# Optimization experiments

Hardware: AMD Instinct MI355X
Metric: run time of the kernel (lower is better)

Reference implementation:

```python
import jax, jax.numpy as jnp
import numpy as np

N_NODES = 50000


def gcn_conv(x, edge_index, W, b):
    """PyG-style GCNConv: add self-loops, symmetric normalization, x@W + bias."""
    N = x.shape[0]
    loop = jnp.arange(N, dtype=edge_index.dtype)
    src = jnp.concatenate([edge_index[0], loop])  # message sources
    dst = jnp.concatenate([edge_index[1], loop])  # aggregation targets
    deg = jax.ops.segment_sum(jnp.ones_like(dst, dtype=x.dtype), dst, num_segments=N)
    dinv = jnp.where(deg > 0, jax.lax.rsqrt(jnp.maximum(deg, 1.0)), 0.0)
    norm = dinv[src] * dinv[dst]  # [E+N]
    h = x @ W  # [N, out] dense transform first (fewer edge-dim FLOPs)
    msg = h[src] * norm[:, None]  # [E+N, out] gathered, normalized messages
    out = jax.ops.segment_sum(msg, dst, num_segments=N)
    return out + b


def setup_inputs() -> dict:
    key = jax.random.key(0)
    k1, k2, k3, k4 = jax.random.split(key, 4)
    x = jax.random.normal(k1, (N_NODES, 256), dtype=jnp.float32)
    edge_index = jax.random.randint(k2, (2, 800000), 0, N_NODES, dtype=jnp.int64)
    W1 = jax.random.normal(k3, (256, 256), dtype=jnp.float32) * (1.0 / np.sqrt(256))
    b1 = jnp.zeros((256,), dtype=jnp.float32)
    W2 = jax.random.normal(k4, (256, 128), dtype=jnp.float32) * (1.0 / np.sqrt(256))
    b2 = jnp.zeros((128,), dtype=jnp.float32)
    return {"x": x, "edge_index": edge_index, "W1": W1, "b1": b1, "W2": W2, "b2": b2}


def reference(x, edge_index, W1, b1, W2, b2):
    h = gcn_conv(x, edge_index, W1, b1)
    h = jax.nn.relu(h)
    return gcn_conv(h, edge_index, W2, b2)
```

## Files before the change

### kernel.cpp

```cpp
#include <hip/hip_runtime.h>

#define N_FEAT_IN 256
#define N_HID 256
#define N_OUT 128

using f32x4 = __attribute__((ext_vector_type(4))) float;
using bf16x8 = __attribute__((ext_vector_type(8))) short;

__device__ inline unsigned short bf16_rne(float f) {
    unsigned u = __builtin_bit_cast(unsigned, f);
    unsigned r = u + 0x7FFFu + ((u >> 16) & 1u);
    return (unsigned short)(r >> 16);
}
__device__ inline float bf16_to_f(unsigned short h) {
    unsigned u = ((unsigned)h) << 16;
    return __builtin_bit_cast(float, u);
}

__global__ void detect_i64_kernel(const int* __restrict__ edges, int* __restrict__ flag) {
    __shared__ int s[256];
    int tid = threadIdx.x;
    int zeros = 0;
    for (int i = tid; i < 2048; i += 256) zeros += (edges[2 * i + 1] == 0) ? 1 : 0;
    s[tid] = zeros;
    __syncthreads();
    for (int off = 128; off; off >>= 1) {
        if (tid < off) s[tid] += s[tid + off];
        __syncthreads();
    }
    if (tid == 0) flag[0] = (s[0] > 1900) ? 1 : 0;
}

__global__ void count_kernel(const void* __restrict__ edges, int E,
                             const int* __restrict__ flag, int* __restrict__ cnt) {
    int e = blockIdx.x * blockDim.x + threadIdx.x;
    if (e >= E) return;
    int d;
    if (flag[0]) {
        d = (int)((const long long*)edges)[(size_t)E + e];
    } else {
        d = ((const int*)edges)[(size_t)E + e];
    }
    atomicAdd(&cnt[d], 1);
}

__global__ __launch_bounds__(256) void scan_block_kernel(
    const int* __restrict__ cnt, int Nn, int* __restrict__ rowp, int* __restrict__ bsum,
    float* __restrict__ dinv) {
    __shared__ int sd[256];
    const int tid = threadIdx.x;
    const int i = blockIdx.x * 256 + tid;
    const int v = (i < Nn) ? cnt[i] : 0;
    if (i < Nn) dinv[i] = rsqrtf((float)(v + 1));
    sd[tid] = v;
    __syncthreads();
    for (int off = 1; off < 256; off <<= 1) {
        int t = (tid >= off) ? sd[tid - off] : 0;
        __syncthreads();
        sd[tid] += t;
        __syncthreads();
    }
    if (i < Nn) rowp[i] = sd[tid] - v;
    if (tid == 255) bsum[blockIdx.x] = sd[255];
}

__global__ __launch_bounds__(256) void scan_top_kernel(
    int* __restrict__ bsum, int Nb, int* __restrict__ rowp, int Nn) {
    __shared__ int sd[256];
    const int tid = threadIdx.x;
    const int v = (tid < Nb) ? bsum[tid] : 0;
    sd[tid] = v;
    __syncthreads();
    for (int off = 1; off < 256; off <<= 1) {
        int t = (tid >= off) ? sd[tid - off] : 0;
        __syncthreads();
        sd[tid] += t;
        __syncthreads();
    }
    if (tid < Nb) bsum[tid] = sd[tid] - v;
    if (tid == 255) rowp[Nn] = sd[255];
}

__global__ __launch_bounds__(256) void scan_add_kernel(
    const int* __restrict__ bsum, int Nn, int* __restrict__ rowp, int* __restrict__ cursor) {
    const int i = blockIdx.x * 256 + threadIdx.x;
    if (i < Nn) {
        const int r = rowp[i] + bsum[i >> 8];
        rowp[i] = r;
        cursor[i] = r;
    }
}

__global__ void fill_kernel(const void* __restrict__ edges, int E,
                            const int* __restrict__ flag,
                            const float* __restrict__ dinv, int* __restrict__ cursor,
                            int2* __restrict__ ce) {
    int e = blockIdx.x * blockDim.x + threadIdx.x;
    if (e >= E) return;
    int s, d;
    if (flag[0]) {
        const long long* p = (const long long*)edges;
        s = (int)p[e];
        d = (int)p[(size_t)E + e];
    } else {
        const int* p = (const int*)edges;
        s = p[e];
        d = p[(size_t)E + e];
    }
    int pos = atomicAdd(&cursor[d], 1);
    float w = dinv[s] * dinv[d];
    ce[pos] = make_int2(s, __builtin_bit_cast(int, w));
}

__global__ __launch_bounds__(256) void splitT_kernel(
    const float* __restrict__ W, int K, int N,
    unsigned short* __restrict__ thi, unsigned short* __restrict__ tlo) {
    int idx = blockIdx.x * 256 + threadIdx.x;
    if (idx >= K * N) return;
    int k = idx / N, n = idx - k * N;
    float f = W[idx];
    unsigned short h = bf16_rne(f);
    unsigned short l = bf16_rne(f - bf16_to_f(h));
    thi[(size_t)n * K + k] = h;
    tlo[(size_t)n * K + k] = l;
}

__global__ __launch_bounds__(256) void gemm_mfma_f32a_kernel(
    const float* __restrict__ Af,
    const unsigned short* __restrict__ Bh, const unsigned short* __restrict__ Bl,
    unsigned short* __restrict__ C, int M, int N, int K) {
    __shared__ char lds[4 * 128 * 64];
    char* As_h = lds;
    char* As_l = lds + 8192;
    char* Bs_h = lds + 16384;
    char* Bs_l = lds + 24576;

    const int tid = threadIdx.x;
    const int lane = tid & 63;
    const int wv = tid >> 6;
    const int wrow = (wv >> 1) * 64;
    const int wcol = (wv & 1) * 64;

    const int srow = tid >> 1;
    const int shalf = tid & 1;

    const long arow_g = (long)blockIdx.y * 128 + srow;
    const bool aval = arow_g < M;
    const int bcol_g = blockIdx.x * 128 + srow;

    const size_t a_base = (size_t)(aval ? arow_g : 0) * K + shalf * 16;
    const size_t b_base = (size_t)bcol_g * K + shalf * 16;

    const int sw = ((srow >> 1) & 3) << 4;
    const int w0 = (srow * 64 + shalf * 32) ^ sw;
    const int w1 = (srow * 64 + shalf * 32 + 16) ^ sw;

    int ra[4], rb[4];
#pragma unroll
    for (int m = 0; m < 4; m++) {
        int r = wrow + m * 16 + (lane & 15);
        ra[m] = (r * 64 + (lane >> 4) * 16) ^ (((r >> 1) & 3) << 4);
        int c = wcol + m * 16 + (lane & 15);
        rb[m] = (c * 64 + (lane >> 4) * 16) ^ (((c >> 1) & 3) << 4);
    }

    f32x4 acc[4][4] = {};

    const int nkt = K >> 5;
    for (int kt = 0; kt < nkt; kt++) {
        const int kb = kt * 32;
        float fa[16];
#pragma unroll
        for (int i = 0; i < 16; i++) fa[i] = 0.f;
        if (aval) {
#pragma unroll
            for (int i = 0; i < 4; i++) {
                float4 f = *(const float4*)(Af + a_base + kb + i * 4);
                fa[i * 4 + 0] = f.x; fa[i * 4 + 1] = f.y;
                fa[i * 4 + 2] = f.z; fa[i * 4 + 3] = f.w;
            }
        }
        bf16x8 vah0, vah1, val0, val1;
#pragma unroll
        for (int i = 0; i < 8; i++) {
            unsigned short hh = bf16_rne(fa[i]);
            unsigned short ll = bf16_rne(fa[i] - bf16_to_f(hh));
            vah0[i] = (short)hh; val0[i] = (short)ll;
            unsigned short hh1 = bf16_rne(fa[8 + i]);
            unsigned short ll1 = bf16_rne(fa[8 + i] - bf16_to_f(hh1));
            vah1[i] = (short)hh1; val1[i] = (short)ll1;
        }
        bf16x8 vbh0 = *(const bf16x8*)(Bh + b_base + kb);
        bf16x8 vbh1 = *(const bf16x8*)(Bh + b_base + kb + 8);
        bf16x8 vbl0 = *(const bf16x8*)(Bl + b_base + kb);
        bf16x8 vbl1 = *(const bf16x8*)(Bl + b_base + kb + 8);
        __syncthreads();
        *(bf16x8*)(As_h + w0) = vah0;  *(bf16x8*)(As_h + w1) = vah1;
        *(bf16x8*)(As_l + w0) = val0;  *(bf16x8*)(As_l + w1) = val1;
        *(bf16x8*)(Bs_h + w0) = vbh0;  *(bf16x8*)(Bs_h + w1) = vbh1;
        *(bf16x8*)(Bs_l + w0) = vbl0;  *(bf16x8*)(Bs_l + w1) = vbl1;
        __syncthreads();
        bf16x8 ah[4], al[4], bh[4], bl[4];
#pragma unroll
        for (int m = 0; m < 4; m++) {
            ah[m] = *(const bf16x8*)(As_h + ra[m]);
            al[m] = *(const bf16x8*)(As_l + ra[m]);
            bh[m] = *(const bf16x8*)(Bs_h + rb[m]);
            bl[m] = *(const bf16x8*)(Bs_l + rb[m]);
        }
#pragma unroll
        for (int m = 0; m < 4; m++)
#pragma unroll
            for (int n = 0; n < 4; n++) {
                acc[m][n] = __builtin_amdgcn_mfma_f32_16x16x32_bf16(ah[m], bh[n], acc[m][n], 0, 0, 0);
                acc[m][n] = __builtin_amdgcn_mfma_f32_16x16x32_bf16(al[m], bh[n], acc[m][n], 0, 0, 0);
                acc[m][n] = __builtin_amdgcn_mfma_f32_16x16x32_bf16(ah[m], bl[n], acc[m][n], 0, 0, 0);
            }
    }

    const int c0 = blockIdx.x * 128 + wcol + (lane & 15);
    const long r0 = (long)blockIdx.y * 128 + wrow + (lane >> 4) * 4;
#pragma unroll
    for (int m = 0; m < 4; m++)
#pragma unroll
        for (int j = 0; j < 4; j++) {
            long r = r0 + m * 16 + j;
            if (r < M) {
#pragma unroll
                for (int n = 0; n < 4; n++)
                    C[(size_t)r * N + c0 + n * 16] = bf16_rne(acc[m][n][j]);
            }
        }
}

__global__ __launch_bounds__(256) void gemm_mfma_kernel(
    const unsigned short* __restrict__ Ah, const unsigned short* __restrict__ Al,
    const unsigned short* __restrict__ Bh, const unsigned short* __restrict__ Bl,
    unsigned short* __restrict__ C, int M, int N, int K) {
    __shared__ char lds[4 * 128 * 64];
    char* As_h = lds;
    char* As_l = lds + 8192;
    char* Bs_h = lds + 16384;
    char* Bs_l = lds + 24576;

    const int tid = threadIdx.x;
    const int lane = tid & 63;
    const int wv = tid >> 6;
    const int wrow = (wv >> 1) * 64;
    const int wcol = (wv & 1) * 64;

    const int srow = tid >> 1;
    const int shalf = tid & 1;

    const long arow_g = (long)blockIdx.y * 128 + srow;
    const bool aval = arow_g < M;
    const int bcol_g = blockIdx.x * 128 + srow;

    const size_t a_base = (size_t)(aval ? arow_g : 0) * K + shalf * 16;
    const size_t b_base = (size_t)bcol_g * K + shalf * 16;

    const int sw = ((srow >> 1) & 3) << 4;
    const int w0 = (srow * 64 + shalf * 32) ^ sw;
    const int w1 = (srow * 64 + shalf * 32 + 16) ^ sw;

    int ra[4], rb[4];
#pragma unroll
    for (int m = 0; m < 4; m++) {
        int r = wrow + m * 16 + (lane & 15);
        ra[m] = (r * 64 + (lane >> 4) * 16) ^ (((r >> 1) & 3) << 4);
        int c = wcol + m * 16 + (lane & 15);
        rb[m] = (c * 64 + (lane >> 4) * 16) ^ (((c >> 1) & 3) << 4);
    }

    f32x4 acc[4][4] = {};
    const bf16x8 zero8 = {0, 0, 0, 0, 0, 0, 0, 0};

    const int nkt = K >> 5;
    for (int kt = 0; kt < nkt; kt++) {
        const int kb = kt * 32;
        bf16x8 vah0 = zero8, vah1 = zero8, val0 = zero8, val1 = zero8;
        if (aval) {
            vah0 = *(const bf16x8*)(Ah + a_base + kb);
            vah1 = *(const bf16x8*)(Ah + a_base + kb + 8);
            val0 = *(const bf16x8*)(Al + a_base + kb);
            val1 = *(const bf16x8*)(Al + a_base + kb + 8);
        }
        bf16x8 vbh0 = *(const bf16x8*)(Bh + b_base + kb);
        bf16x8 vbh1 = *(const bf16x8*)(Bh + b_base + kb + 8);
        bf16x8 vbl0 = *(const bf16x8*)(Bl + b_base + kb);
        bf16x8 vbl1 = *(const bf16x8*)(Bl + b_base + kb + 8);
        __syncthreads();
        *(bf16x8*)(As_h + w0) = vah0;  *(bf16x8*)(As_h + w1) = vah1;
        *(bf16x8*)(As_l + w0) = val0;  *(bf16x8*)(As_l + w1) = val1;
        *(bf16x8*)(Bs_h + w0) = vbh0;  *(bf16x8*)(Bs_h + w1) = vbh1;
        *(bf16x8*)(Bs_l + w0) = vbl0;  *(bf16x8*)(Bs_l + w1) = vbl1;
        __syncthreads();
        bf16x8 ah[4], al[4], bh[4], bl[4];
#pragma unroll
        for (int m = 0; m < 4; m++) {
            ah[m] = *(const bf16x8*)(As_h + ra[m]);
            al[m] = *(const bf16x8*)(As_l + ra[m]);
            bh[m] = *(const bf16x8*)(Bs_h + rb[m]);
            bl[m] = *(const bf16x8*)(Bs_l + rb[m]);
        }
#pragma unroll
        for (int m = 0; m < 4; m++)
#pragma unroll
            for (int n = 0; n < 4; n++) {
                acc[m][n] = __builtin_amdgcn_mfma_f32_16x16x32_bf16(ah[m], bh[n], acc[m][n], 0, 0, 0);
                acc[m][n] = __builtin_amdgcn_mfma_f32_16x16x32_bf16(al[m], bh[n], acc[m][n], 0, 0, 0);
                acc[m][n] = __builtin_amdgcn_mfma_f32_16x16x32_bf16(ah[m], bl[n], acc[m][n], 0, 0, 0);
            }
    }

    const int c0 = blockIdx.x * 128 + wcol + (lane & 15);
    const long r0 = (long)blockIdx.y * 128 + wrow + (lane >> 4) * 4;
#pragma unroll
    for (int m = 0; m < 4; m++)
#pragma unroll
        for (int j = 0; j < 4; j++) {
            long r = r0 + m * 16 + j;
            if (r < M) {
#pragma unroll
                for (int n = 0; n < 4; n++)
                    C[(size_t)r * N + c0 + n * 16] = bf16_rne(acc[m][n][j]);
            }
        }
}

template <int C, bool RELU, bool SPLIT>
__global__ __launch_bounds__(256) void agg_kernel(
    const unsigned short* __restrict__ h, const int* __restrict__ rowp,
    const int2* __restrict__ ce,
    const float* __restrict__ dinv, const float* __restrict__ bias,
    float* __restrict__ out,
    unsigned short* __restrict__ ohi, unsigned short* __restrict__ olo, int Nn) {
    constexpr int VEC = C / 64;
    static_assert(VEC == 2 || VEC == 4, "C must be 128 or 256");
    const int lane = threadIdx.x & 63;
    const int wv = threadIdx.x >> 6;
    const int node0 = blockIdx.x * 4 + wv;
    if (node0 >= Nn) return;
    const int node = __builtin_amdgcn_readfirstlane(node0);
    const float di = dinv[node];
    const int coff = lane * VEC;
    const unsigned short* __restrict__ hc = h + coff;
    float acc[VEC];

    auto loadrow = [&](int row, float v[VEC]) {
        const unsigned short* r = hc + (size_t)row * C;
        if constexpr (VEC == 4) {
            ushort4 t = *(const ushort4*)r;
            v[0] = bf16_to_f(t.x); v[1] = bf16_to_f(t.y);
            v[2] = bf16_to_f(t.z); v[3] = bf16_to_f(t.w);
        } else {
            ushort2 t = *(const ushort2*)r;
            v[0] = bf16_to_f(t.x); v[1] = bf16_to_f(t.y);
        }
    };

    {
        float v[VEC];
        loadrow(node, v);
#pragma unroll
        for (int j = 0; j < VEC; j++) acc[j] = di * di * v[j];
    }

    const int s = rowp[node];
    const int e = rowp[node + 1];
    for (int base = s; base < e; base += 64) {
        const int m = min(64, e - base);
        int myc = 0, myn = 0;
        if (lane < m) {
            int2 p = ce[base + lane];
            myc = p.x;
            myn = p.y;
        }
        int j = 0;
        for (; j + 4 <= m; j += 4) {
            const int c0 = __builtin_amdgcn_readlane(myc, j);
            const int c1 = __builtin_amdgcn_readlane(myc, j + 1);
            const int c2 = __builtin_amdgcn_readlane(myc, j + 2);
            const int c3 = __builtin_amdgcn_readlane(myc, j + 3);
            const float w0 = __builtin_bit_cast(float, __builtin_amdgcn_readlane(myn, j));
            const float w1 = __builtin_bit_cast(float, __builtin_amdgcn_readlane(myn, j + 1));
            const float w2 = __builtin_bit_cast(float, __builtin_amdgcn_readlane(myn, j + 2));
            const float w3 = __builtin_bit_cast(float, __builtin_amdgcn_readlane(myn, j + 3));
            float v0[VEC], v1[VEC], v2[VEC], v3[VEC];
            loadrow(c0, v0);
            loadrow(c1, v1);
            loadrow(c2, v2);
            loadrow(c3, v3);
#pragma unroll
            for (int q = 0; q < VEC; q++)
                acc[q] += w0 * v0[q] + w1 * v1[q] + w2 * v2[q] + w3 * v3[q];
        }
        for (; j < m; ++j) {
            const int c0 = __builtin_amdgcn_readlane(myc, j);
            const float w0 = __builtin_bit_cast(float, __builtin_amdgcn_readlane(myn, j));
            float v0[VEC];
            loadrow(c0, v0);
#pragma unroll
            for (int q = 0; q < VEC; q++) acc[q] += w0 * v0[q];
        }
    }

    {
        const float* bv = bias + coff;
#pragma unroll
        for (int j = 0; j < VEC; j++) {
            acc[j] += bv[j];
            if (RELU) acc[j] = fmaxf(acc[j], 0.f);
        }
    }
    if constexpr (SPLIT) {
        if constexpr (VEC == 4) {
            ushort4 hh, ll;
            hh.x = bf16_rne(acc[0]); ll.x = bf16_rne(acc[0] - bf16_to_f(hh.x));
            hh.y = bf16_rne(acc[1]); ll.y = bf16_rne(acc[1] - bf16_to_f(hh.y));
            hh.z = bf16_rne(acc[2]); ll.z = bf16_rne(acc[2] - bf16_to_f(hh.z));
            hh.w = bf16_rne(acc[3]); ll.w = bf16_rne(acc[3] - bf16_to_f(hh.w));
            *(ushort4*)(ohi + (size_t)node * C + coff) = hh;
            *(ushort4*)(olo + (size_t)node * C + coff) = ll;
        } else {
            ushort2 hh, ll;
            hh.x = bf16_rne(acc[0]); ll.x = bf16_rne(acc[0] - bf16_to_f(hh.x));
            hh.y = bf16_rne(acc[1]); ll.y = bf16_rne(acc[1] - bf16_to_f(hh.y));
            *(ushort2*)(ohi + (size_t)node * C + coff) = hh;
            *(ushort2*)(olo + (size_t)node * C + coff) = ll;
        }
    } else {
        float* o = out + (size_t)node * C + coff;
        if constexpr (VEC == 4) {
            *(float4*)o = make_float4(acc[0], acc[1], acc[2], acc[3]);
        } else {
            *(float2*)o = make_float2(acc[0], acc[1]);
        }
    }
}

extern "C" void kernel_launch(void* const* d_in, const int* in_sizes, int n_in,
                              void* d_out, int out_size, void* d_ws, size_t ws_size,
                              hipStream_t stream) {
    const float* x = (const float*)d_in[0];
    const void* edges = d_in[1];
    const float* W1 = (const float*)d_in[2];
    const float* b1 = (const float*)d_in[3];
    const float* W2 = (const float*)d_in[4];
    const float* b2 = (const float*)d_in[5];
    float* out = (float*)d_out;

    const int Nn = in_sizes[0] / N_FEAT_IN;
    const int E = in_sizes[1] / 2;

    char* w = (char*)d_ws;
    size_t off = 0;
    auto alloc = [&](size_t bytes) -> void* {
        void* p = (void*)(w + off);
        off += (bytes + 255) & ~(size_t)255;
        return p;
    };
    int* flag = (int*)alloc(sizeof(int));
    int* cnt = (int*)alloc((size_t)Nn * 4);
    int* rowp = (int*)alloc(((size_t)Nn + 1) * 4);
    int* cursor = (int*)alloc((size_t)Nn * 4);
    int* bsum = (int*)alloc(1024 * 4);
    int2* ce = (int2*)alloc((size_t)E * 8);
    float* dinv = (float*)alloc((size_t)Nn * 4);
    unsigned short* w1hi = (unsigned short*)alloc((size_t)N_FEAT_IN * N_HID * 2);
    unsigned short* w1lo = (unsigned short*)alloc((size_t)N_FEAT_IN * N_HID * 2);
    unsigned short* w2hi = (unsigned short*)alloc((size_t)N_HID * N_OUT * 2);
    unsigned short* w2lo = (unsigned short*)alloc((size_t)N_HID * N_OUT * 2);
    unsigned short* a1hi = (unsigned short*)alloc((size_t)Nn * N_HID * 2);
    unsigned short* a1lo = (unsigned short*)alloc((size_t)Nn * N_HID * 2);
    unsigned short* h = (unsigned short*)alloc((size_t)Nn * N_HID * 2);

    hipMemsetAsync(cnt, 0, (size_t)Nn * 4, stream);
    detect_i64_kernel<<<1, 256, 0, stream>>>((const int*)edges, flag);
    const int eb = (E + 255) / 256;
    count_kernel<<<eb, 256, 0, stream>>>(edges, E, flag, cnt);
    const int nb = (Nn + 255) / 256;
    scan_block_kernel<<<nb, 256, 0, stream>>>(cnt, Nn, rowp, bsum, dinv);
    scan_top_kernel<<<1, 256, 0, stream>>>(bsum, nb, rowp, Nn);
    scan_add_kernel<<<nb, 256, 0, stream>>>(bsum, Nn, rowp, cursor);
    fill_kernel<<<eb, 256, 0, stream>>>(edges, E, flag, dinv, cursor, ce);

    splitT_kernel<<<(N_FEAT_IN * N_HID + 255) / 256, 256, 0, stream>>>(W1, N_FEAT_IN, N_HID, w1hi, w1lo);
    splitT_kernel<<<(N_HID * N_OUT + 255) / 256, 256, 0, stream>>>(W2, N_HID, N_OUT, w2hi, w2lo);

    dim3 g1(N_HID / 128, (Nn + 127) / 128);
    gemm_mfma_f32a_kernel<<<g1, 256, 0, stream>>>(x, w1hi, w1lo, h, Nn, N_HID, N_FEAT_IN);
    agg_kernel<N_HID, true, true><<<(Nn + 3) / 4, 256, 0, stream>>>(
        h, rowp, ce, dinv, b1, nullptr, a1hi, a1lo, Nn);

    dim3 g2(N_OUT / 128, (Nn + 127) / 128);
    gemm_mfma_kernel<<<g2, 256, 0, stream>>>(a1hi, a1lo, w2hi, w2lo, h, Nn, N_OUT, N_HID);
    agg_kernel<N_OUT, false, false><<<(Nn + 3) / 4, 256, 0, stream>>>(
        h, rowp, ce, dinv, b2, out, nullptr, nullptr, Nn);
}
```

Baseline: 250.2 us.

## Replace direct CSR fill with two-pass coarse bucket sort by destination

The single scatter kernel that atomically placed each edge into its CSR slot is replaced by two passes. The first groups edges into 512-node destination buckets, using a shared-memory histogram and one global atomic per bucket per block. The second reads the bucketed edges and does the per-node atomic scatter with much better locality. The aim is to cut random global atomics and scattered writes, at the cost of an extra E-sized intermediate buffer, one more pass over it, and one more kernel launch.

Result: slower. 297.7 us (+19.0%).

```diff
diff --git a/kernel.cpp b/kernel.cpp
--- a/kernel.cpp
+++ b/kernel.cpp
@@ -3,6 +3,7 @@
 #define N_FEAT_IN 256
 #define N_HID 256
 #define N_OUT 128
+#define NPB_SHIFT 9
 
 using f32x4 = __attribute__((ext_vector_type(4))) float;
 using bf16x8 = __attribute__((ext_vector_type(8))) short;
@@ -82,33 +83,59 @@
 }
 
 __global__ __launch_bounds__(256) void scan_add_kernel(
-    const int* __restrict__ bsum, int Nn, int* __restrict__ rowp, int* __restrict__ cursor) {
+    const int* __restrict__ bsum, int Nn, int* __restrict__ rowp,
+    int* __restrict__ cursor, int* __restrict__ bucketCur) {
     const int i = blockIdx.x * 256 + threadIdx.x;
     if (i < Nn) {
         const int r = rowp[i] + bsum[i >> 8];
         rowp[i] = r;
         cursor[i] = r;
-    }
-}
-
-__global__ void fill_kernel(const void* __restrict__ edges, int E,
-                            const int* __restrict__ flag,
-                            const float* __restrict__ dinv, int* __restrict__ cursor,
-                            int2* __restrict__ ce) {
-    int e = blockIdx.x * blockDim.x + threadIdx.x;
-    if (e >= E) return;
-    int s, d;
-    if (flag[0]) {
-        const long long* p = (const long long*)edges;
-        s = (int)p[e];
-        d = (int)p[(size_t)E + e];
-    } else {
-        const int* p = (const int*)edges;
-        s = p[e];
-        d = p[(size_t)E + e];
-    }
-    int pos = atomicAdd(&cursor[d], 1);
-    float w = dinv[s] * dinv[d];
+        if ((i & ((1 << NPB_SHIFT) - 1)) == 0) bucketCur[i >> NPB_SHIFT] = r;
+    }
+}
+
+__global__ __launch_bounds__(256) void bucketA_kernel(
+    const void* __restrict__ edges, int E, const int* __restrict__ flag,
+    int* __restrict__ bucketCur, int2* __restrict__ bucketBuf, int NB) {
+    __shared__ int hist[128];
+    __shared__ int base[128];
+    const int tid = threadIdx.x;
+    if (tid < NB) hist[tid] = 0;
+    __syncthreads();
+    const int e = blockIdx.x * 256 + tid;
+    int s = 0, d = 0, b = 0, rank = 0;
+    const bool val = e < E;
+    if (val) {
+        if (flag[0]) {
+            const long long* p = (const long long*)edges;
+            s = (int)p[e];
+            d = (int)p[(size_t)E + e];
+        } else {
+            const int* p = (const int*)edges;
+            s = p[e];
+            d = p[(size_t)E + e];
+        }
+        b = d >> NPB_SHIFT;
+        rank = atomicAdd(&hist[b], 1);
+    }
+    __syncthreads();
+    if (tid < NB) {
+        const int c = hist[tid];
+        base[tid] = c ? atomicAdd(&bucketCur[tid], c) : 0;
+    }
+    __syncthreads();
+    if (val) bucketBuf[base[b] + rank] = make_int2(s, d);
+}
+
+__global__ __launch_bounds__(256) void bucketB_kernel(
+    const int2* __restrict__ bucketBuf, int E, const float* __restrict__ dinv,
+    int* __restrict__ cursor, int2* __restrict__ ce) {
+    const int i = blockIdx.x * 256 + threadIdx.x;
+    if (i >= E) return;
+    const int2 p = bucketBuf[i];
+    const int s = p.x, d = p.y;
+    const int pos = atomicAdd(&cursor[d], 1);
+    const float w = dinv[s] * dinv[d];
     ce[pos] = make_int2(s, __builtin_bit_cast(int, w));
 }
 
@@ -452,6 +479,7 @@
 
     const int Nn = in_sizes[0] / N_FEAT_IN;
     const int E = in_sizes[1] / 2;
+    const int NB = (Nn + (1 << NPB_SHIFT) - 1) >> NPB_SHIFT;
 
     char* w = (char*)d_ws;
     size_t off = 0;
@@ -465,6 +493,8 @@
     int* rowp = (int*)alloc(((size_t)Nn + 1) * 4);
     int* cursor = (int*)alloc((size_t)Nn * 4);
     int* bsum = (int*)alloc(1024 * 4);
+    int* bucketCur = (int*)alloc(128 * 4);
+    int2* bucketBuf = (int2*)alloc((size_t)E * 8);
     int2* ce = (int2*)alloc((size_t)E * 8);
     float* dinv = (float*)alloc((size_t)Nn * 4);
     unsigned short* w1hi = (unsigned short*)alloc((size_t)N_FEAT_IN * N_HID * 2);
@@ -482,8 +512,9 @@
     const int nb = (Nn + 255) / 256;
     scan_block_kernel<<<nb, 256, 0, stream>>>(cnt, Nn, rowp, bsum, dinv);
     scan_top_kernel<<<1, 256, 0, stream>>>(bsum, nb, rowp, Nn);
-    scan_add_kernel<<<nb, 256, 0, stream>>>(bsum, Nn, rowp, cursor);
-    fill_kernel<<<eb, 256, 0, stream>>>(edges, E, flag, dinv, cursor, ce);
+    scan_add_kernel<<<nb, 256, 0, stream>>>(bsum, Nn, rowp, cursor, bucketCur);
+    bucketA_kernel<<<eb, 256, 0, stream>>>(edges, E, flag, bucketCur, bucketBuf, NB);
+    bucketB_kernel<<<eb, 256, 0, stream>>>(bucketBuf, E, dinv, cursor, ce);
 
     splitT_kernel<<<(N_FEAT_IN * N_HID + 255) / 256, 256, 0, stream>>>(W1, N_FEAT_IN, N_HID, w1hi, w1lo);
     splitT_kernel<<<(N_HID * N_OUT + 255) / 256, 256, 0, stream>>>(W2, N_HID, N_OUT, w2hi, w2lo);
```
